# Performance work log

Measured on AMD Instinct MI355X. Metric: run time of the kernel, lower is better.

## Reference

```python
import jax, jax.numpy as jnp
import numpy as np

BETA = 0.25
K = 1024   # num_codebook_vectors
D = 256    # latent_dim


def setup_inputs() -> dict:
    key = jax.random.key(0)
    k1, k2 = jax.random.split(key)
    z = jax.random.normal(k1, (16, D, 64, 64), dtype=jnp.float32)
    # embedding initialized uniform(-1/K, 1/K) as in the torch module
    emb = jax.random.uniform(k2, (K, D), dtype=jnp.float32, minval=-1.0 / K, maxval=1.0 / K)
    return {"z": z, "emb": emb}


def reference(z, emb):
    sg = jax.lax.stop_gradient
    # NCHW -> NHWC
    z_nhwc = jnp.transpose(z, (0, 2, 3, 1))            # [B,H,W,D]
    zf = z_nhwc.reshape(-1, D)                          # [N,D]
    # squared euclidean distances: ||z||^2 + ||e||^2 - 2 z e^T
    d = (jnp.sum(zf * zf, axis=1, keepdims=True)
         + jnp.sum(emb * emb, axis=1)
         - 2.0 * jnp.matmul(zf, emb.T))                 # [N,K]
    min_encoding_indices = jnp.argmin(d, axis=1)        # [N] int
    z_q = emb[min_encoding_indices].reshape(z_nhwc.shape)  # [B,H,W,D]
    # loss exactly as in source (first term is zero in value, faithful)
    loss = (jnp.mean((sg(z_nhwc) - z_nhwc) ** 2)
            + BETA * jnp.mean((z_q - sg(z_nhwc)) ** 2))
    # straight-through estimator
    z_q_st = z_nhwc + sg(z_q - z_nhwc)
    out = jnp.transpose(z_q_st, (0, 3, 1, 2))           # NHWC -> NCHW
    return out, min_encoding_indices, loss
```

## Files before the change

### kernel.cpp

```cpp
#include <hip/hip_runtime.h>

#define DD 256
#define KK 1024
#define HW 4096
#define NROWSZ 65536
#define OUT_Z 16777216
#define OUT_IDX OUT_Z
#define OUT_LOSS (OUT_Z + NROWSZ)

#define MARGIN 3.0e-4f

#define WS_ESQ   0
#define WS_EH    4096
#define WS_HLIST 528384
#define WS_HCNT  790528
#define WS_LSUM  790536
#define WS_EMBT  791552
#define WS_HZ    1840128

typedef _Float16 f16x8 __attribute__((ext_vector_type(8)));
typedef float f32x4 __attribute__((ext_vector_type(4)));
union U16x8 { uint4 u; f16x8 h; };
typedef unsigned long long u64;

static __device__ __forceinline__ u64 umin64(u64 a, u64 b) { return a < b ? a : b; }
static __device__ __forceinline__ unsigned fkey(float s) {
    unsigned b = __float_as_uint(s);
    unsigned flip = (unsigned)((int)b >> 31) | 0x80000000u;
    return b ^ flip;
}
static __device__ __forceinline__ float funkey(unsigned k) {
    unsigned b = (k & 0x80000000u) ? (k ^ 0x80000000u) : ~k;
    return __uint_as_float(b);
}
static __device__ __forceinline__ unsigned pk16(float a, float b) {
    _Float16 ha = (_Float16)a, hb = (_Float16)b;
    return (unsigned)__builtin_bit_cast(unsigned short, ha)
         | ((unsigned)__builtin_bit_cast(unsigned short, hb) << 16);
}

__global__ void vq_prep(const float* __restrict__ emb, float* __restrict__ esq,
                        uint2* __restrict__ eh2, int* __restrict__ hcnt,
                        double* __restrict__ lsum, float* __restrict__ embT,
                        int use_embT)
{
    const int bid = blockIdx.x;
    const int t = threadIdx.x;
    if (bid == 0 && t == 0) { *hcnt = 0; *lsum = 0.0; }

    if (bid < 4) {
        int k = bid * 256 + t;
        const float* e = emb + (size_t)k * DD;
        float blk[2];
#pragma unroll
        for (int b2 = 0; b2 < 2; ++b2) {
            const float* p = e + b2 * 128;
            float r[8];
#pragma unroll
            for (int j = 0; j < 8; ++j) r[j] = __fmul_rn(p[j], p[j]);
            for (int i = 8; i < 128; i += 8) {
#pragma unroll
                for (int j = 0; j < 8; ++j)
                    r[j] = __fadd_rn(r[j], __fmul_rn(p[i + j], p[i + j]));
            }
            blk[b2] = __fadd_rn(__fadd_rn(__fadd_rn(r[0], r[1]), __fadd_rn(r[2], r[3])),
                                __fadd_rn(__fadd_rn(r[4], r[5]), __fadd_rn(r[6], r[7])));
        }
        esq[k] = __fadd_rn(blk[0], blk[1]);
    } else if (bid < 20) {
        int tid = (bid - 4) * 256 + t;
        const float4* e4 = (const float4*)emb;
#pragma unroll
        for (int i = 0; i < 16; ++i) {
            int idx = i * 4096 + tid;
            float4 v = e4[idx];
            eh2[idx] = make_uint2(pk16(v.x, v.y), pk16(v.z, v.w));
        }
    } else {
        if (!use_embT) return;
        int u = bid - 20;
        int k = u * 64 + (t >> 2);
        int c = t & 3;
        const float4* e4 = (const float4*)(emb + (size_t)k * DD);
#pragma unroll
        for (int i = 0; i < 16; ++i) {
            float4 v = e4[c * 16 + i];
            int d = c * 64 + i * 4;
            embT[(size_t)(d + 0) * KK + k] = v.x;
            embT[(size_t)(d + 1) * KK + k] = v.y;
            embT[(size_t)(d + 2) * KK + k] = v.z;
            embT[(size_t)(d + 3) * KK + k] = v.w;
        }
    }
}

__launch_bounds__(256, 2)
__global__ void vq_score(const float* __restrict__ z, const float* __restrict__ emb,
                         const _Float16* __restrict__ eh, const float* __restrict__ esq,
                         float* __restrict__ out, int* __restrict__ hlist,
                         int* __restrict__ hcnt, double* __restrict__ lsum,
                         float* __restrict__ hz, int hzcap)
{
    __shared__ __align__(16) float zf[64 * 264];
    __shared__ uint2 cand[64][4];
    __shared__ int idxs[64];
    __shared__ float wsum[4];

    const int t = threadIdx.x;
    const int lane = t & 63;
    const int w = t >> 6;
    const int col = lane & 15;
    const int quad = lane >> 4;

    const int n0 = blockIdx.x * 64;
    const int b = n0 >> 12;
    const int hw0 = n0 & (HW - 1);
    const float* zbase = z + (size_t)b * DD * HW;

    {
        const int r = t & 63, dg = t >> 6;
        const float* src = zbase + hw0 + r + (size_t)(dg * 64) * HW;
        float* dst = &zf[r * 264 + dg * 64];
#pragma unroll 4
        for (int i = 0; i < 16; ++i) {
            float4 v;
            v.x = src[(size_t)(4 * i + 0) * HW];
            v.y = src[(size_t)(4 * i + 1) * HW];
            v.z = src[(size_t)(4 * i + 2) * HW];
            v.w = src[(size_t)(4 * i + 3) * HW];
            *(float4*)&dst[i * 4] = v;
        }
    }
    __syncthreads();

    U16x8 af[4][8];
#pragma unroll
    for (int nt = 0; nt < 4; ++nt)
#pragma unroll
        for (int ds = 0; ds < 8; ++ds) {
            const float* p = &zf[(nt * 16 + col) * 264 + ds * 32 + quad * 8];
            float4 x0 = *(const float4*)p;
            float4 x1 = *(const float4*)(p + 4);
            af[nt][ds].u = make_uint4(pk16(x0.x, x0.y), pk16(x0.z, x0.w),
                                      pk16(x1.x, x1.y), pk16(x1.z, x1.w));
        }

    unsigned t1[16], t2[16];
#pragma unroll
    for (int i = 0; i < 16; ++i) { t1[i] = 0xFFFFFFFFu; t2[i] = 0xFFFFFFFFu; }

    const uint4* ehq = (const uint4*)eh;
    const int cbase = w * 256;
    for (int ct = 0; ct < 16; ++ct) {
        const int code = cbase + ct * 16 + col;
        const float eq = esq[code];
        const uint4* bp = ehq + (size_t)code * 32 + quad;
        f32x4 acc[4];
#pragma unroll
        for (int nt = 0; nt < 4; ++nt) acc[nt] = (f32x4)0.0f;
#pragma unroll
        for (int ds = 0; ds < 8; ++ds) {
            U16x8 bf;
            bf.u = bp[ds * 4];
#pragma unroll
            for (int nt = 0; nt < 4; ++nt)
                acc[nt] = __builtin_amdgcn_mfma_f32_16x16x32_f16(af[nt][ds].h, bf.h,
                                                                 acc[nt], 0, 0, 0);
        }
#pragma unroll
        for (int nt = 0; nt < 4; ++nt)
#pragma unroll
            for (int r = 0; r < 4; ++r) {
                float s = __fsub_rn(eq, __fmul_rn(2.0f, acc[nt][r]));
                unsigned key = (fkey(s) & 0xFFFFFC00u) | (unsigned)code;
                int mi = nt * 4 + r;
                unsigned mx = max(t1[mi], key);
                t1[mi] = min(t1[mi], key);
                t2[mi] = min(t2[mi], mx);
            }
    }

#pragma unroll
    for (int mi = 0; mi < 16; ++mi) {
        unsigned a = t1[mi], bb = t2[mi];
#pragma unroll
        for (int off = 1; off < 16; off <<= 1) {
            unsigned o1 = __shfl_xor(a, off, 16);
            unsigned o2 = __shfl_xor(bb, off, 16);
            unsigned mx = max(a, o1);
            a = min(a, o1);
            bb = min(min(bb, o2), mx);
        }
        if (col == 0) {
            int row = (mi >> 2) * 16 + quad * 4 + (mi & 3);
            cand[row][w] = make_uint2(a, bb);
        }
    }
    __syncthreads();

    if (t < 64) {
        uint2 c0 = cand[t][0];
        unsigned a = c0.x, bb = c0.y;
#pragma unroll
        for (int ww = 1; ww < 4; ++ww) {
            uint2 c = cand[t][ww];
            unsigned mx = max(a, c.x);
            a = min(a, c.x);
            bb = min(min(bb, c.y), mx);
        }
        float s1 = funkey(a & 0xFFFFFC00u);
        float s2 = funkey(bb & 0xFFFFFC00u);
        int k1 = (int)(a & 1023u);
        if (__fsub_rn(s2, s1) > MARGIN) {
            idxs[t] = k1;
            out[OUT_IDX + n0 + t] = (float)k1;
        } else {
            int pos = atomicAdd(hcnt, 1);
            hlist[pos] = n0 + t;
            idxs[t] = -2 - pos;
        }
    }
    __syncthreads();

    {
        const int rr = t & 63;
        const int dg = t >> 6;
        int idx = idxs[rr];
        float lacc = 0.f;
        if (idx >= 0) {
            const float* erow = emb + (size_t)idx * DD;
            const float* zrow = &zf[rr * 264];
            float* oc = out + (size_t)b * DD * HW + hw0 + rr;
#pragma unroll 4
            for (int dd = 0; dd < 64; ++dd) {
                int d = dg * 64 + dd;
                float e = erow[d];
                float zv = zrow[d];
                oc[(size_t)d * HW] = e;
                float df = e - zv;
                lacc = fmaf(df, df, lacc);
            }
        } else {
            int pos = -2 - idx;
            if (pos < hzcap) {
                float4* dst = (float4*)(hz + (size_t)pos * DD + dg * 64);
                const float4* srcv = (const float4*)(&zf[rr * 264 + dg * 64]);
#pragma unroll
                for (int i = 0; i < 16; ++i) dst[i] = srcv[i];
            }
        }
#pragma unroll
        for (int off = 32; off > 0; off >>= 1) lacc += __shfl_down(lacc, off, 64);
        if (lane == 0) wsum[w] = lacc;
    }
    __syncthreads();
    if (t == 0) {
        double tot = (double)wsum[0] + (double)wsum[1] + (double)wsum[2] + (double)wsum[3];
        atomicAdd(lsum, tot);
    }
}

template<int USET>
static __device__ __forceinline__ void dot_codes(const float4* __restrict__ embT4,
                                                 const float4* __restrict__ emb4,
                                                 const float4* __restrict__ zb4,
                                                 int t, float (&acc_)[8][4])
{
#pragma unroll 2
    for (int dc = 0; dc < 64; ++dc) {
        float4 e0, e1, e2, e3;
        if (USET) {
            e0 = embT4[(size_t)(dc * 4 + 0) * 256 + t];
            e1 = embT4[(size_t)(dc * 4 + 1) * 256 + t];
            e2 = embT4[(size_t)(dc * 4 + 2) * 256 + t];
            e3 = embT4[(size_t)(dc * 4 + 3) * 256 + t];
        } else {
            float4 a0 = emb4[(size_t)(4 * t + 0) * 64 + dc];
            float4 a1 = emb4[(size_t)(4 * t + 1) * 64 + dc];
            float4 a2 = emb4[(size_t)(4 * t + 2) * 64 + dc];
            float4 a3 = emb4[(size_t)(4 * t + 3) * 64 + dc];
            e0 = make_float4(a0.x, a1.x, a2.x, a3.x);
            e1 = make_float4(a0.y, a1.y, a2.y, a3.y);
            e2 = make_float4(a0.z, a1.z, a2.z, a3.z);
            e3 = make_float4(a0.w, a1.w, a2.w, a3.w);
        }
#pragma unroll
        for (int j = 0; j < 8; ++j) {
            float4 zv = zb4[j * 64 + dc];
            acc_[j][0] = fmaf(zv.x, e0.x, acc_[j][0]);
            acc_[j][1] = fmaf(zv.x, e0.y, acc_[j][1]);
            acc_[j][2] = fmaf(zv.x, e0.z, acc_[j][2]);
            acc_[j][3] = fmaf(zv.x, e0.w, acc_[j][3]);
            acc_[j][0] = fmaf(zv.y, e1.x, acc_[j][0]);
            acc_[j][1] = fmaf(zv.y, e1.y, acc_[j][1]);
            acc_[j][2] = fmaf(zv.y, e1.z, acc_[j][2]);
            acc_[j][3] = fmaf(zv.y, e1.w, acc_[j][3]);
            acc_[j][0] = fmaf(zv.z, e2.x, acc_[j][0]);
            acc_[j][1] = fmaf(zv.z, e2.y, acc_[j][1]);
            acc_[j][2] = fmaf(zv.z, e2.z, acc_[j][2]);
            acc_[j][3] = fmaf(zv.z, e2.w, acc_[j][3]);
            acc_[j][0] = fmaf(zv.w, e3.x, acc_[j][0]);
            acc_[j][1] = fmaf(zv.w, e3.y, acc_[j][1]);
            acc_[j][2] = fmaf(zv.w, e3.z, acc_[j][2]);
            acc_[j][3] = fmaf(zv.w, e3.w, acc_[j][3]);
        }
    }
}

__launch_bounds__(256)
__global__ void vq_hard(const float* __restrict__ z, const float* __restrict__ emb,
                        const float* __restrict__ embT, const float* __restrict__ esq,
                        const float* __restrict__ hz, const int* __restrict__ hlist,
                        const int* __restrict__ hcnt, float* __restrict__ out,
                        double* __restrict__ lsum, int hzcap, int use_embT)
{
    __shared__ __align__(16) float zbuf[8 * 256];
    __shared__ float chains[8][16];
    __shared__ float zq_s[8];
    __shared__ int rows_s[8];
    __shared__ int idx_s[8];
    __shared__ u64 red[4][8];
    __shared__ float wsum[4];

    const int t = threadIdx.x;
    const int lane = t & 63;
    const int w = t >> 6;
    const int count = *hcnt;
    float lacc = 0.f;

    const float4* embT4 = (const float4*)embT;
    const float4* emb4 = (const float4*)emb;
    const float4* hz4 = (const float4*)hz;
    const float4* zb4 = (const float4*)zbuf;
    const float4 eqv4 = ((const float4*)esq)[t];
    const float eqa[4] = {eqv4.x, eqv4.y, eqv4.z, eqv4.w};

    for (int g = blockIdx.x; g * 8 < count; g += gridDim.x) {
        __syncthreads();
        if (t < 8) {
            int p = g * 8 + t;
            rows_s[t] = (p < count) ? hlist[p] : -1;
        }
        __syncthreads();

        {
            const int j = t >> 5, dpos = t & 31;
            const int pos = g * 8 + j;
            const int r = rows_s[j];
            float4 v0 = make_float4(0.f, 0.f, 0.f, 0.f), v1 = v0;
            if (r >= 0) {
                if (pos < hzcap) {
                    v0 = hz4[(size_t)pos * 64 + dpos * 2];
                    v1 = hz4[(size_t)pos * 64 + dpos * 2 + 1];
                } else {
                    const float* zp = z + (size_t)(r >> 12) * (DD * HW) + (r & (HW - 1));
                    const int d0 = dpos * 8;
                    v0.x = zp[(size_t)(d0 + 0) * HW];
                    v0.y = zp[(size_t)(d0 + 1) * HW];
                    v0.z = zp[(size_t)(d0 + 2) * HW];
                    v0.w = zp[(size_t)(d0 + 3) * HW];
                    v1.x = zp[(size_t)(d0 + 4) * HW];
                    v1.y = zp[(size_t)(d0 + 5) * HW];
                    v1.z = zp[(size_t)(d0 + 6) * HW];
                    v1.w = zp[(size_t)(d0 + 7) * HW];
                }
            }
            *(float4*)&zbuf[j * 256 + dpos * 8] = v0;
            *(float4*)&zbuf[j * 256 + dpos * 8 + 4] = v1;
        }
        __syncthreads();

        if (t < 128) {
            int j = t >> 4, c = t & 15, b2 = c >> 3, jj = c & 7;
            const float* p = &zbuf[j * 256];
            int base = b2 * 128 + jj;
            float v = p[base];
            float acc = __fmul_rn(v, v);
            for (int i = 1; i < 16; ++i) {
                float u = p[base + i * 8];
                acc = __fadd_rn(acc, __fmul_rn(u, u));
            }
            chains[j][c] = acc;
        }
        __syncthreads();
        if (t < 8) {
            const float* c = chains[t];
            float b0 = __fadd_rn(__fadd_rn(__fadd_rn(c[0], c[1]), __fadd_rn(c[2], c[3])),
                                 __fadd_rn(__fadd_rn(c[4], c[5]), __fadd_rn(c[6], c[7])));
            float b1 = __fadd_rn(__fadd_rn(__fadd_rn(c[8], c[9]), __fadd_rn(c[10], c[11])),
                                 __fadd_rn(__fadd_rn(c[12], c[13]), __fadd_rn(c[14], c[15])));
            zq_s[t] = __fadd_rn(b0, b1);
        }
        __syncthreads();

        float acc_[8][4];
#pragma unroll
        for (int j = 0; j < 8; ++j)
#pragma unroll
            for (int kk = 0; kk < 4; ++kk) acc_[j][kk] = 0.0f;

        if (use_embT) dot_codes<1>(embT4, emb4, zb4, t, acc_);
        else          dot_codes<0>(embT4, emb4, zb4, t, acc_);

#pragma unroll
        for (int j = 0; j < 8; ++j) {
            u64 m = ~0ull;
#pragma unroll
            for (int kk = 0; kk < 4; ++kk) {
                float s = __fsub_rn(__fadd_rn(zq_s[j], eqa[kk]),
                                    __fmul_rn(2.0f, acc_[j][kk]));
                u64 p = ((u64)__float_as_uint(s) << 32) | (unsigned)(4 * t + kk);
                m = umin64(m, p);
            }
#pragma unroll
            for (int off = 1; off < 64; off <<= 1)
                m = umin64(m, __shfl_xor(m, off, 64));
            if (lane == 0) red[w][j] = m;
        }
        __syncthreads();
        if (t < 8) {
            u64 m = umin64(umin64(red[0][t], red[1][t]), umin64(red[2][t], red[3][t]));
            int ki = (int)(m & 0xffffffffu);
            idx_s[t] = ki;
            int r = rows_s[t];
            if (r >= 0) out[OUT_IDX + r] = (float)ki;
        }
        __syncthreads();

        for (int p = t; p < 2048; p += 256) {
            int j = p >> 8, d = p & 255;
            int r = rows_s[j];
            if (r >= 0) {
                float e = emb[(size_t)idx_s[j] * DD + d];
                size_t off = (size_t)(r >> 12) * (DD * HW) + (size_t)d * HW + (r & (HW - 1));
                float zv = zbuf[j * 256 + d];
                out[off] = e;
                float df = e - zv;
                lacc = fmaf(df, df, lacc);
            }
        }
    }

#pragma unroll
    for (int off = 32; off > 0; off >>= 1) lacc += __shfl_down(lacc, off, 64);
    if (lane == 0) wsum[w] = lacc;
    __syncthreads();
    if (t == 0) {
        double tot = (double)wsum[0] + (double)wsum[1] + (double)wsum[2] + (double)wsum[3];
        if (tot != 0.0) atomicAdd(lsum, tot);
    }
}

__global__ void vq_final(const double* __restrict__ lsum, float* __restrict__ out)
{
    out[OUT_LOSS] = (float)(0.25 * (lsum[0] / (double)OUT_Z));
}

extern "C" void kernel_launch(void* const* d_in, const int* in_sizes, int n_in,
                              void* d_out, int out_size, void* d_ws, size_t ws_size,
                              hipStream_t stream)
{
    const float* z = (const float*)d_in[0];
    const float* emb = (const float*)d_in[1];
    float* out = (float*)d_out;
    char* w = (char*)d_ws;

    float* esq = (float*)(w + WS_ESQ);
    _Float16* eh = (_Float16*)(w + WS_EH);
    uint2* eh2 = (uint2*)(w + WS_EH);
    int* hlist = (int*)(w + WS_HLIST);
    int* hcnt = (int*)(w + WS_HCNT);
    double* lsum = (double*)(w + WS_LSUM);
    float* embT = (float*)(w + WS_EMBT);
    float* hz = (float*)(w + WS_HZ);

    int use_embT = (ws_size >= (size_t)WS_EMBT + (size_t)DD * KK * sizeof(float)) ? 1 : 0;
    int hzcap = 0;
    if (ws_size > (size_t)WS_HZ) {
        size_t c = (ws_size - (size_t)WS_HZ) / ((size_t)DD * sizeof(float));
        hzcap = (c > (size_t)NROWSZ) ? NROWSZ : (int)c;
    }

    vq_prep<<<dim3(36), dim3(256), 0, stream>>>(emb, esq, eh2, hcnt, lsum, embT, use_embT);
    vq_score<<<dim3(1024), dim3(256), 0, stream>>>(z, emb, eh, esq, out, hlist, hcnt, lsum,
                                                   hz, hzcap);
    vq_hard<<<dim3(512), dim3(256), 0, stream>>>(z, emb, embT, esq, hz, hlist, hcnt, out,
                                                 lsum, hzcap, use_embT);
    vq_final<<<dim3(1), dim3(1), 0, stream>>>(lsum, out);
}
```

Measured before the change: 253.7 us.

## Stage fp16 codebook tiles through LDS with double buffering in score kernel

```diff
diff --git a/kernel.cpp b/kernel.cpp
--- a/kernel.cpp
+++ b/kernel.cpp
@@ -8,7 +8,7 @@
 #define OUT_IDX OUT_Z
 #define OUT_LOSS (OUT_Z + NROWSZ)
 
-#define MARGIN 3.0e-4f
+#define MARGIN 4.5e-4f
 
 #define WS_ESQ   0
 #define WS_EH    4096
@@ -24,19 +24,15 @@
 typedef unsigned long long u64;
 
 static __device__ __forceinline__ u64 umin64(u64 a, u64 b) { return a < b ? a : b; }
-static __device__ __forceinline__ unsigned fkey(float s) {
-    unsigned b = __float_as_uint(s);
-    unsigned flip = (unsigned)((int)b >> 31) | 0x80000000u;
-    return b ^ flip;
-}
-static __device__ __forceinline__ float funkey(unsigned k) {
-    unsigned b = (k & 0x80000000u) ? (k ^ 0x80000000u) : ~k;
-    return __uint_as_float(b);
-}
 static __device__ __forceinline__ unsigned pk16(float a, float b) {
     _Float16 ha = (_Float16)a, hb = (_Float16)b;
     return (unsigned)__builtin_bit_cast(unsigned short, ha)
          | ((unsigned)__builtin_bit_cast(unsigned short, hb) << 16);
+}
+static __device__ __forceinline__ void gl_lds16(const void* g, void* l) {
+    __builtin_amdgcn_global_load_lds(
+        (const __attribute__((address_space(1))) unsigned int*)g,
+        (__attribute__((address_space(3))) unsigned int*)l, 16, 0, 0);
 }
 
 __global__ void vq_prep(const float* __restrict__ emb, float* __restrict__ esq,
@@ -101,16 +97,21 @@
                          int* __restrict__ hcnt, double* __restrict__ lsum,
                          float* __restrict__ hz, int hzcap)
 {
-    __shared__ __align__(16) float zf[64 * 264];
-    __shared__ uint2 cand[64][4];
-    __shared__ int idxs[64];
-    __shared__ float wsum[4];
+    __shared__ __align__(16) char smem[70928];
+    char* ebufc = smem + 32768;
+    float* esq_s = (float*)(smem + 65536);
+    uint2 (*cand)[2] = (uint2 (*)[2])(smem + 69632);
+    int* idxs = (int*)(smem + 70656);
+    float* wsum = (float*)(smem + 70912);
+    float* er = (float*)smem;
 
     const int t = threadIdx.x;
     const int lane = t & 63;
     const int w = t >> 6;
     const int col = lane & 15;
     const int quad = lane >> 4;
+    const int wr = w >> 1;
+    const int wc = w & 1;
 
     const int n0 = blockIdx.x * 64;
     const int b = n0 >> 12;
@@ -119,69 +120,88 @@
 
     {
         const int r = t & 63, dg = t >> 6;
-        const float* src = zbase + hw0 + r + (size_t)(dg * 64) * HW;
-        float* dst = &zf[r * 264 + dg * 64];
-#pragma unroll 4
-        for (int i = 0; i < 16; ++i) {
-            float4 v;
-            v.x = src[(size_t)(4 * i + 0) * HW];
-            v.y = src[(size_t)(4 * i + 1) * HW];
-            v.z = src[(size_t)(4 * i + 2) * HW];
-            v.w = src[(size_t)(4 * i + 3) * HW];
-            *(float4*)&dst[i * 4] = v;
-        }
-    }
-    __syncthreads();
-
-    U16x8 af[4][8];
-#pragma unroll
-    for (int nt = 0; nt < 4; ++nt)
-#pragma unroll
-        for (int ds = 0; ds < 8; ++ds) {
-            const float* p = &zf[(nt * 16 + col) * 264 + ds * 32 + quad * 8];
-            float4 x0 = *(const float4*)p;
-            float4 x1 = *(const float4*)(p + 4);
-            af[nt][ds].u = make_uint4(pk16(x0.x, x0.y), pk16(x0.z, x0.w),
-                                      pk16(x1.x, x1.y), pk16(x1.z, x1.w));
-        }
-
-    unsigned t1[16], t2[16];
-#pragma unroll
-    for (int i = 0; i < 16; ++i) { t1[i] = 0xFFFFFFFFu; t2[i] = 0xFFFFFFFFu; }
-
-    const uint4* ehq = (const uint4*)eh;
-    const int cbase = w * 256;
-    for (int ct = 0; ct < 16; ++ct) {
-        const int code = cbase + ct * 16 + col;
-        const float eq = esq[code];
-        const uint4* bp = ehq + (size_t)code * 32 + quad;
-        f32x4 acc[4];
-#pragma unroll
-        for (int nt = 0; nt < 4; ++nt) acc[nt] = (f32x4)0.0f;
+        const float* src = zbase + hw0 + r;
+#pragma unroll
+        for (int i = 0; i < 8; ++i) {
+            const int d0 = dg * 64 + i * 8;
+            float v0 = src[(size_t)(d0 + 0) * HW];
+            float v1 = src[(size_t)(d0 + 1) * HW];
+            float v2 = src[(size_t)(d0 + 2) * HW];
+            float v3 = src[(size_t)(d0 + 3) * HW];
+            float v4 = src[(size_t)(d0 + 4) * HW];
+            float v5 = src[(size_t)(d0 + 5) * HW];
+            float v6 = src[(size_t)(d0 + 6) * HW];
+            float v7 = src[(size_t)(d0 + 7) * HW];
+            uint4 pk = make_uint4(pk16(v0, v1), pk16(v2, v3), pk16(v4, v5), pk16(v6, v7));
+            *(uint4*)(smem + r * 512 + ((d0 * 2) ^ ((r & 7) << 4))) = pk;
+        }
+        esq_s[t] = esq[t];
+        esq_s[256 + t] = esq[256 + t];
+        esq_s[512 + t] = esq[512 + t];
+        esq_s[768 + t] = esq[768 + t];
+    }
+    __syncthreads();
+
+    const char* ehB = (const char*)eh;
+    auto stage_tile = [&](int tt, int bufsel) {
+#pragma unroll
+        for (int i = 0; i < 4; ++i) {
+            int pbyte = (w * 4 + i) * 1024 + lane * 16;
+            int soff = pbyte ^ (((pbyte >> 9) & 7) << 4);
+            gl_lds16(ehB + (size_t)tt * 16384 + soff,
+                     ebufc + bufsel * 16384 + (w * 4 + i) * 1024);
+        }
+    };
+    stage_tile(0, 0);
+
+    U16x8 af[2][8];
+#pragma unroll
+    for (int nt = 0; nt < 2; ++nt)
+#pragma unroll
+        for (int ds = 0; ds < 8; ++ds)
+            af[nt][ds].u = *(const uint4*)(smem + (wr * 32 + nt * 16 + col) * 512
+                                           + ((ds * 64 + quad * 16) ^ ((col & 7) << 4)));
+    __syncthreads();
+
+    unsigned t1[8], t2[8];
+#pragma unroll
+    for (int i = 0; i < 8; ++i) { t1[i] = 0xFFFFFFFFu; t2[i] = 0xFFFFFFFFu; }
+
+    const int cbyte = (wc * 16 + col) * 512;
+    const int swzc = (col & 7) << 4;
+
+    for (int tt = 0; tt < 32; ++tt) {
+        const int cur = tt & 1;
+        if (tt + 1 < 32) stage_tile(tt + 1, cur ^ 1);
+
+        const char* bbuf = ebufc + cur * 16384 + cbyte;
+        const int code = tt * 32 + wc * 16 + col;
+        const float eq1 = 1.0f + esq_s[code];
+
+        f32x4 acc0 = (f32x4)0.0f, acc1 = (f32x4)0.0f;
 #pragma unroll
         for (int ds = 0; ds < 8; ++ds) {
             U16x8 bf;
-            bf.u = bp[ds * 4];
-#pragma unroll
-            for (int nt = 0; nt < 4; ++nt)
-                acc[nt] = __builtin_amdgcn_mfma_f32_16x16x32_f16(af[nt][ds].h, bf.h,
-                                                                 acc[nt], 0, 0, 0);
-        }
-#pragma unroll
-        for (int nt = 0; nt < 4; ++nt)
-#pragma unroll
-            for (int r = 0; r < 4; ++r) {
-                float s = __fsub_rn(eq, __fmul_rn(2.0f, acc[nt][r]));
-                unsigned key = (fkey(s) & 0xFFFFFC00u) | (unsigned)code;
-                int mi = nt * 4 + r;
-                unsigned mx = max(t1[mi], key);
-                t1[mi] = min(t1[mi], key);
-                t2[mi] = min(t2[mi], mx);
-            }
-    }
-
-#pragma unroll
-    for (int mi = 0; mi < 16; ++mi) {
+            bf.u = *(const uint4*)(bbuf + ((ds * 64 + quad * 16) ^ swzc));
+            acc0 = __builtin_amdgcn_mfma_f32_16x16x32_f16(af[0][ds].h, bf.h, acc0, 0, 0, 0);
+            acc1 = __builtin_amdgcn_mfma_f32_16x16x32_f16(af[1][ds].h, bf.h, acc1, 0, 0, 0);
+        }
+#pragma unroll
+        for (int r = 0; r < 4; ++r) {
+            float s0 = fmaf(-2.0f, acc0[r], eq1);
+            unsigned k0 = (__float_as_uint(s0) & 0xFFFFFC00u) | (unsigned)code;
+            t2[r] = min(t2[r], max(t1[r], k0));
+            t1[r] = min(t1[r], k0);
+            float s1 = fmaf(-2.0f, acc1[r], eq1);
+            unsigned k1 = (__float_as_uint(s1) & 0xFFFFFC00u) | (unsigned)code;
+            t2[4 + r] = min(t2[4 + r], max(t1[4 + r], k1));
+            t1[4 + r] = min(t1[4 + r], k1);
+        }
+        __syncthreads();
+    }
+
+#pragma unroll
+    for (int mi = 0; mi < 8; ++mi) {
         unsigned a = t1[mi], bb = t2[mi];
 #pragma unroll
         for (int off = 1; off < 16; off <<= 1) {
@@ -191,25 +211,18 @@
             a = min(a, o1);
             bb = min(min(bb, o2), mx);
         }
-        if (col == 0) {
-            int row = (mi >> 2) * 16 + quad * 4 + (mi & 3);
-            cand[row][w] = make_uint2(a, bb);
-        }
+        if (col == 0)
+            cand[wr * 32 + (mi >> 2) * 16 + quad * 4 + (mi & 3)][wc] = make_uint2(a, bb);
     }
     __syncthreads();
 
     if (t < 64) {
-        uint2 c0 = cand[t][0];
-        unsigned a = c0.x, bb = c0.y;
-#pragma unroll
-        for (int ww = 1; ww < 4; ++ww) {
-            uint2 c = cand[t][ww];
-            unsigned mx = max(a, c.x);
-            a = min(a, c.x);
-            bb = min(min(bb, c.y), mx);
-        }
-        float s1 = funkey(a & 0xFFFFFC00u);
-        float s2 = funkey(bb & 0xFFFFFC00u);
+        uint2 c0 = cand[t][0], c1 = cand[t][1];
+        unsigned mx = max(c0.x, c1.x);
+        unsigned a = min(c0.x, c1.x);
+        unsigned bb = min(min(c0.y, c1.y), mx);
+        float s1 = __uint_as_float(a & 0xFFFFFC00u);
+        float s2 = __uint_as_float(bb & 0xFFFFFC00u);
         int k1 = (int)(a & 1023u);
         if (__fsub_rn(s2, s1) > MARGIN) {
             idxs[t] = k1;
@@ -223,30 +236,61 @@
     __syncthreads();
 
     {
-        const int rr = t & 63;
-        const int dg = t >> 6;
+        const int row = t >> 2;
+        const int cl = t & 3;
+        int idx = idxs[row];
+        if (idx >= 0) {
+            const float4* e4 = (const float4*)(emb + (size_t)idx * DD);
+#pragma unroll
+            for (int i = 0; i < 16; ++i) {
+                int ch = i * 4 + cl;
+                int d0 = ch * 4;
+                float4 v = e4[ch];
+                *(float4*)&er[row * 256 + ((d0 + row * 4) & 255)] = v;
+            }
+        }
+    }
+    __syncthreads();
+
+    {
+        const int rr = t & 63, dg = t >> 6;
         int idx = idxs[rr];
         float lacc = 0.f;
+        const float* zcol = zbase + hw0 + rr;
         if (idx >= 0) {
-            const float* erow = emb + (size_t)idx * DD;
-            const float* zrow = &zf[rr * 264];
             float* oc = out + (size_t)b * DD * HW + hw0 + rr;
 #pragma unroll 4
-            for (int dd = 0; dd < 64; ++dd) {
-                int d = dg * 64 + dd;
-                float e = erow[d];
-                float zv = zrow[d];
-                oc[(size_t)d * HW] = e;
-                float df = e - zv;
-                lacc = fmaf(df, df, lacc);
+            for (int i = 0; i < 16; ++i) {
+                int d0 = dg * 64 + i * 4;
+                float4 e4 = *(const float4*)&er[rr * 256 + ((d0 + rr * 4) & 255)];
+                float z0 = zcol[(size_t)(d0 + 0) * HW];
+                float z1 = zcol[(size_t)(d0 + 1) * HW];
+                float z2 = zcol[(size_t)(d0 + 2) * HW];
+                float z3 = zcol[(size_t)(d0 + 3) * HW];
+                oc[(size_t)(d0 + 0) * HW] = e4.x;
+                oc[(size_t)(d0 + 1) * HW] = e4.y;
+                oc[(size_t)(d0 + 2) * HW] = e4.z;
+                oc[(size_t)(d0 + 3) * HW] = e4.w;
+                float df;
+                df = e4.x - z0; lacc = fmaf(df, df, lacc);
+                df = e4.y - z1; lacc = fmaf(df, df, lacc);
+                df = e4.z - z2; lacc = fmaf(df, df, lacc);
+                df = e4.w - z3; lacc = fmaf(df, df, lacc);
             }
         } else {
             int pos = -2 - idx;
             if (pos < hzcap) {
-                float4* dst = (float4*)(hz + (size_t)pos * DD + dg * 64);
-                const float4* srcv = (const float4*)(&zf[rr * 264 + dg * 64]);
-#pragma unroll
-                for (int i = 0; i < 16; ++i) dst[i] = srcv[i];
+                float4* dst = (float4*)(hz + (size_t)pos * DD);
+#pragma unroll 4
+                for (int i = 0; i < 16; ++i) {
+                    int d0 = dg * 64 + i * 4;
+                    float4 v;
+                    v.x = zcol[(size_t)(d0 + 0) * HW];
+                    v.y = zcol[(size_t)(d0 + 1) * HW];
+                    v.z = zcol[(size_t)(d0 + 2) * HW];
+                    v.w = zcol[(size_t)(d0 + 3) * HW];
+                    dst[d0 >> 2] = v;
+                }
             }
         }
 #pragma unroll
@@ -484,7 +528,7 @@
     vq_prep<<<dim3(36), dim3(256), 0, stream>>>(emb, esq, eh2, hcnt, lsum, embT, use_embT);
     vq_score<<<dim3(1024), dim3(256), 0, stream>>>(z, emb, eh, esq, out, hlist, hcnt, lsum,
                                                    hz, hzcap);
-    vq_hard<<<dim3(512), dim3(256), 0, stream>>>(z, emb, embT, esq, hz, hlist, hcnt, out,
-                                                 lsum, hzcap, use_embT);
+    vq_hard<<<dim3(1024), dim3(256), 0, stream>>>(z, emb, embT, esq, hz, hlist, hcnt, out,
+                                                  lsum, hzcap, use_embT);
     vq_final<<<dim3(1), dim3(1), 0, stream>>>(lsum, out);
 }
```

After: 278.3 us. +9.7%, slower.
